# Kernel optimization log

Measured on AMD Instinct MI355X. Metric: run time of the kernel, lower is better.

Reference implementation:

```python
import jax, jax.numpy as jnp
import numpy as np

N_HEAD = 8
DROP_RATE = 0.1


def setup_inputs() -> dict:
    key = jax.random.key(0)
    k1, k2, k3 = jax.random.split(key, 3)
    n, c, h, w = 16, 512, 32, 32
    return {
        "x": jax.random.normal(k1, (n, c, h, w), jnp.float32),
        "qkv_w": jax.random.normal(k2, (3 * c, c), jnp.float32) * 0.02,
        "qkv_b": jnp.zeros((3 * c,), jnp.float32),
        "out_w": jax.random.normal(k3, (c, c), jnp.float32) * 0.02,
        "out_b": jnp.zeros((c,), jnp.float32),
        "dropout_enabled": 0,
    }


def reference(x, qkv_w, qkv_b, out_w, out_b, dropout_enabled):
    n, c, h, w = x.shape
    hd = c // N_HEAD  # head dim
    # fused QKV 1x1 conv == per-pixel matmul: [n, 3c, h, w]
    qkv = jnp.einsum('oc,nchw->nohw', qkv_w, x) + qkv_b[None, :, None, None]
    # [n, 3*n_head, hd, h*w] -> [n, 3*n_head, h*w, hd]
    qkv = jnp.swapaxes(qkv.reshape(n, N_HEAD * 3, hd, h * w), 2, 3)
    q, k, v = jnp.split(qkv, 3, axis=1)  # each [n, n_head, hw, hd]
    scale = hd ** (-0.25)
    att = jax.nn.softmax((q * scale) @ (jnp.swapaxes(k, 2, 3) * scale), axis=3)
    y = jnp.swapaxes(att @ v, 2, 3).reshape(n, c, h, w)
    y = jnp.einsum('oc,nchw->nohw', out_w, y) + out_b[None, :, None, None]
    # Dropout2d: drops whole (n, c) channel maps
    rate = DROP_RATE * dropout_enabled
    keep = jax.random.bernoulli(jax.random.key(42), 1.0 - rate, shape=(n, c))
    y = y * keep[..., None, None] / (1.0 - rate)
    return x + y
```

## Files before the change

kernel.cpp:

```cpp
#include <hip/hip_runtime.h>

typedef short bf16x8 __attribute__((ext_vector_type(8)));
typedef float f32x4 __attribute__((ext_vector_type(4)));
typedef float f32x16 __attribute__((ext_vector_type(16)));

#define MFMA16(a,b,c) __builtin_amdgcn_mfma_f32_16x16x32_bf16((a),(b),(c),0,0,0)
#define MFMA32(a,b,c) __builtin_amdgcn_mfma_f32_32x32x16_bf16((a),(b),(c),0,0,0)

static __device__ __forceinline__ unsigned short f2bf(float f){
  unsigned u; __builtin_memcpy(&u, &f, 4);
  u += 0x7fffu + ((u >> 16) & 1u);
  return (unsigned short)(u >> 16);
}

static __device__ __forceinline__ unsigned cvtpk(float lo, float hi){
  unsigned r;
  asm volatile("v_cvt_pk_bf16_f32 %0, %1, %2" : "=v"(r) : "v"(lo), "v"(hi));
  return r;
}
static __device__ __forceinline__ void pl32swap(unsigned &a, unsigned &b){
  asm volatile("v_permlane32_swap_b32 %0, %1" : "+v"(a), "+v"(b));
}

static __device__ __forceinline__ void gload_lds16(const void* g, void* l) {
  __builtin_amdgcn_global_load_lds(
      (__attribute__((address_space(1))) void*)g,
      (__attribute__((address_space(3))) void*)l, 16, 0, 0);
}

__global__ __launch_bounds__(256) void transpose_cvt(
    const float* __restrict__ in, unsigned short* __restrict__ out,
    const float* __restrict__ qkv_w, const float* __restrict__ out_w,
    unsigned short* __restrict__ wq, unsigned short* __restrict__ wo)
{
  __shared__ unsigned short tile[32][33];
  if (blockIdx.x >= 32) {
    const int b = (blockIdx.x - 32) + 8 * (blockIdx.y + 16 * blockIdx.z);
    const int i = b * 512 + threadIdx.x * 2;
    float2 v; unsigned short* dst;
    if (i < 786432) { v = *(const float2*)&qkv_w[i]; dst = &wq[i]; }
    else { v = *(const float2*)&out_w[i - 786432]; dst = &wo[i - 786432]; }
    dst[0] = f2bf(v.x); dst[1] = f2bf(v.y);
    return;
  }
  const long base = (long)blockIdx.z * 512 * 1024;
  const int t = threadIdx.x, tx = t & 31, ty = t >> 5;
  const int c0 = blockIdx.x * 32, r0 = blockIdx.y * 32;
  const float* ib = in + base;
#pragma unroll
  for (int i = 0; i < 4; ++i)
    tile[ty + i * 8][tx] = f2bf(ib[(long)(r0 + ty + i * 8) * 1024 + c0 + tx]);
  __syncthreads();
  unsigned short* ob = out + base;
#pragma unroll
  for (int i = 0; i < 4; ++i)
    ob[(long)(c0 + ty + i * 8) * 512 + r0 + tx] = tile[tx][ty + i * 8];
}

__global__ __launch_bounds__(256, 2) void gemm_qkv(
    const unsigned short* __restrict__ A, const unsigned short* __restrict__ B,
    unsigned short* __restrict__ qkvout, const float* __restrict__ bias)
{
  const int M = 1024, K = 512;
  __shared__ unsigned short SM[4][128 * 64];
  const int t = threadIdx.x, lane = t & 63, wv = t >> 6;
  const int quad = lane >> 4, ln = lane & 15;

  const int L = blockIdx.x + 12 * blockIdx.y + 96 * blockIdx.z;
  const int v = (L & 7) * 192 + (L >> 3);
  const int m0 = ((v / 12) & 7) * 128, n0 = (v % 12) * 128;
  const long zb = v / 96;
  A += zb * (long)M * K;

  const int srow = wv * 32 + (lane >> 3);
  const int scol = ((lane & 7) * 8) ^ ((lane >> 3) * 8);

  auto stage = [&](int kt, unsigned short* Ad, unsigned short* Bd) {
#pragma unroll
    for (int i = 0; i < 4; ++i) {
      gload_lds16(&A[(long)(m0 + srow + i * 8) * K + kt + scol],
                  &Ad[(wv * 32 + i * 8) * 64]);
      gload_lds16(&B[(long)(n0 + srow + i * 8) * K + kt + scol],
                  &Bd[(wv * 32 + i * 8) * 64]);
    }
  };

  f32x4 zero = {0.f, 0.f, 0.f, 0.f};
  f32x4 acc[4][4];
#pragma unroll
  for (int i = 0; i < 4; ++i)
#pragma unroll
    for (int j = 0; j < 4; ++j) acc[i][j] = zero;

  const int wm = (wv & 1) * 64, wn = (wv >> 1) * 64;
  const int rsw = (ln & 7) * 8;

  stage(0, SM[0], SM[2]);
  __syncthreads();
  for (int kt8 = 0; kt8 < 8; ++kt8) {
    const int cur = kt8 & 1;
    if (kt8 < 7) stage((kt8 + 1) * 64, SM[cur ^ 1], SM[2 + (cur ^ 1)]);
    const unsigned short* As = SM[cur];
    const unsigned short* Bs = SM[2 + cur];
#pragma unroll
    for (int kk = 0; kk < 64; kk += 32) {
      bf16x8 a[4], b[4];
#pragma unroll
      for (int i = 0; i < 4; ++i)
        a[i] = *(const bf16x8*)&As[(wm + i * 16 + ln) * 64 + ((kk + quad * 8) ^ rsw)];
#pragma unroll
      for (int j = 0; j < 4; ++j)
        b[j] = *(const bf16x8*)&Bs[(wn + j * 16 + ln) * 64 + ((kk + quad * 8) ^ rsw)];
#pragma unroll
      for (int i = 0; i < 4; ++i)
#pragma unroll
        for (int j = 0; j < 4; ++j)
          acc[i][j] = MFMA16(a[i], b[j], acc[i][j]);
    }
    __syncthreads();
  }

  const int part = n0 >> 9;
  if (part < 2) {
    const float qs = (part == 0) ? 0.18033688f : 1.0f;
    unsigned short (*T)[136] = (unsigned short(*)[136])&SM[0][0];
#pragma unroll
    for (int j = 0; j < 4; ++j) {
      const int oo = wn + j * 16 + ln;
      const float bb = bias[n0 + oo];
#pragma unroll
      for (int i = 0; i < 4; ++i) {
        const int pp = wm + i * 16 + quad * 4;
        f32x4 vv = acc[i][j];
#pragma unroll
        for (int r = 0; r < 4; ++r)
          T[pp + r][oo] = f2bf((vv[r] + bb) * qs);
      }
    }
    __syncthreads();
    unsigned short* qb = qkvout + (long)part * 8388608;
#pragma unroll
    for (int it = 0; it < 8; ++it) {
      const int idx = it * 256 + t;
      const int p = idx >> 4, c0 = (idx & 15) * 8;
      const int og = n0 + c0;
      const int h = (og >> 6) & 7, d = og & 63;
      bf16x8 val = *(const bf16x8*)&T[p][c0];
      *(bf16x8*)&qb[((long)(zb * 8 + h) * 1024 + m0 + p) * 64 + d] = val;
    }
  } else {
#pragma unroll
    for (int j = 0; j < 4; ++j) {
      const int o = n0 + wn + j * 16 + ln;
      const float bb = bias[o];
#pragma unroll
      for (int i = 0; i < 4; ++i) {
        const int p = m0 + wm + i * 16 + quad * 4;
        const long cidx = ((long)zb * 512 + (o - 1024)) * 1024 + p;
        f32x4 vv = acc[i][j];
        ushort4 st;
        st.x = f2bf(vv[0] + bb); st.y = f2bf(vv[1] + bb);
        st.z = f2bf(vv[2] + bb); st.w = f2bf(vv[3] + bb);
        *(ushort4*)&qkvout[16777216 + cidx] = st;
      }
    }
  }
}

__global__ __launch_bounds__(256, 2) void gemm_out(
    const unsigned short* __restrict__ A, const unsigned short* __restrict__ B,
    float* __restrict__ C, const float* __restrict__ bias,
    const float* __restrict__ xin, const int* __restrict__ de_ptr)
{
  const int M = 1024, K = 512;
  __shared__ unsigned short SM[4][128 * 64];
  const int t = threadIdx.x, lane = t & 63, wv = t >> 6;
  const int quad = lane >> 4, ln = lane & 15;

  const int L = blockIdx.x + 4 * blockIdx.y + 32 * blockIdx.z;
  const int v = (L & 7) * 64 + (L >> 3);
  const int m0 = ((v >> 2) & 7) * 128, n0 = (v & 3) * 128;
  const long zb = v >> 5;
  A += zb * (long)M * K;
  C += zb * 512l * M;
  xin += zb * 512l * M;

  const int srow = wv * 32 + (lane >> 3);
  const int scol = ((lane & 7) * 8) ^ ((lane >> 3) * 8);

  auto stage = [&](int kt, unsigned short* Ad, unsigned short* Bd) {
#pragma unroll
    for (int i = 0; i < 4; ++i) {
      gload_lds16(&A[(long)(m0 + srow + i * 8) * K + kt + scol],
                  &Ad[(wv * 32 + i * 8) * 64]);
      gload_lds16(&B[(long)(n0 + srow + i * 8) * K + kt + scol],
                  &Bd[(wv * 32 + i * 8) * 64]);
    }
  };

  f32x4 zero = {0.f, 0.f, 0.f, 0.f};
  f32x4 acc[4][4];
#pragma unroll
  for (int i = 0; i < 4; ++i)
#pragma unroll
    for (int j = 0; j < 4; ++j) acc[i][j] = zero;

  const int wm = (wv & 1) * 64, wn = (wv >> 1) * 64;
  const int rsw = (ln & 7) * 8;

  stage(0, SM[0], SM[2]);
  __syncthreads();
  for (int kt8 = 0; kt8 < 8; ++kt8) {
    const int cur = kt8 & 1;
    if (kt8 < 7) stage((kt8 + 1) * 64, SM[cur ^ 1], SM[2 + (cur ^ 1)]);
    const unsigned short* As = SM[cur];
    const unsigned short* Bs = SM[2 + cur];
#pragma unroll
    for (int kk = 0; kk < 64; kk += 32) {
      bf16x8 a[4], b[4];
#pragma unroll
      for (int i = 0; i < 4; ++i)
        a[i] = *(const bf16x8*)&As[(wm + i * 16 + ln) * 64 + ((kk + quad * 8) ^ rsw)];
#pragma unroll
      for (int j = 0; j < 4; ++j)
        b[j] = *(const bf16x8*)&Bs[(wn + j * 16 + ln) * 64 + ((kk + quad * 8) ^ rsw)];
#pragma unroll
      for (int i = 0; i < 4; ++i)
#pragma unroll
        for (int j = 0; j < 4; ++j)
          acc[i][j] = MFMA16(a[i], b[j], acc[i][j]);
    }
    __syncthreads();
  }

  float dscale = 1.0f / (1.0f - 0.1f * (float)de_ptr[0]);

#pragma unroll
  for (int j = 0; j < 4; ++j) {
    int o = n0 + wn + j * 16 + ln;
    float bb = bias[o];
#pragma unroll
    for (int i = 0; i < 4; ++i) {
      int p = m0 + wm + i * 16 + quad * 4;
      long cidx = (long)o * M + p;
      f32x4 vv = acc[i][j];
      float4 rx = *(const float4*)&xin[cidx];
      float4 st;
      st.x = rx.x + (vv[0] + bb) * dscale;
      st.y = rx.y + (vv[1] + bb) * dscale;
      st.z = rx.z + (vv[2] + bb) * dscale;
      st.w = rx.w + (vv[3] + bb) * dscale;
      *(float4*)&C[cidx] = st;
    }
  }
}

__global__ __launch_bounds__(512, 2) void attn_kernel(
    const unsigned short* __restrict__ q_pd, const unsigned short* __restrict__ k_pd,
    const unsigned short* __restrict__ v_cp, unsigned short* __restrict__ y_pc)
{
  __shared__ unsigned short Ks[2][128 * 64];
  __shared__ unsigned short Vs[2][64 * 128];
  const int t = threadIdx.x, lane = t & 63, wv = t >> 6;
  const int l31 = lane & 31, bh8 = (lane >> 5) * 8;
  const int qt = blockIdx.y >> 5;
  const int nh = blockIdx.x * 32 + (blockIdx.y & 31);
  const int n = nh >> 3, h = nh & 7;
  const int q0 = qt * 512;

  bf16x8 qa[2][4];
#pragma unroll
  for (int qg = 0; qg < 2; ++qg) {
    const unsigned short* qb =
        q_pd + ((long)nh * 1024 + q0 + wv * 64 + qg * 32 + l31) * 64;
#pragma unroll
    for (int ds = 0; ds < 4; ++ds)
      qa[qg][ds] = *(const bf16x8*)(qb + ds * 16 + bh8);
  }

  f32x16 zacc;
#pragma unroll
  for (int r = 0; r < 16; ++r) zacc[r] = 0.f;
  f32x16 o_acc[2][2];
  o_acc[0][0] = zacc; o_acc[0][1] = zacc; o_acc[1][0] = zacc; o_acc[1][1] = zacc;
  float l_acc[2] = {0.f, 0.f};

  const unsigned short* kg0 = k_pd + (long)nh * 1024 * 64;
  const unsigned short* vg0 = v_cp + ((long)n * 512 + h * 64) * 1024;

  const int krow = lane >> 3;
  const int kcol = ((lane & 7) * 8) ^ ((lane >> 3) * 8);
  const int vrow = lane >> 4;
  const int rsw = (lane & 7) * 8;
  const int vrsw = (l31 & 15) * 8;

  auto stage_kv = [&](int c, int buf) {
    const unsigned short* kg = kg0 + (long)c * 128 * 64;
    const unsigned short* vg = vg0 + c * 128;
    unsigned short* KsD = Ks[buf];
    unsigned short* VsD = Vs[buf];
#pragma unroll
    for (int i = 0; i < 2; ++i) {
      const int vr = ((wv & 1) * 8) + i * 4 + vrow;
      const int vcol = ((lane & 15) ^ vr) * 8;
      gload_lds16(kg + (long)(wv * 16 + i * 8 + krow) * 64 + kcol,
                  &KsD[(wv * 16 + i * 8) * 64]);
      gload_lds16(vg + (long)(wv * 8 + i * 4 + vrow) * 1024 + vcol,
                  &VsD[(wv * 8 + i * 4) * 128]);
    }
  };

  stage_kv(0, 0);

  union U { bf16x8 v; unsigned u[4]; };
  auto sm_pack = [&](const f32x16& sv, bf16x8* paq, float& lac) {
    float e[16];
#pragma unroll
    for (int r = 0; r < 16; ++r) e[r] = __builtin_amdgcn_exp2f(sv[r]);
    float a0 = e[0] + e[1],  a1 = e[2] + e[3],  a2 = e[4] + e[5],  a3 = e[6] + e[7];
    float a4 = e[8] + e[9],  a5 = e[10] + e[11], a6 = e[12] + e[13], a7 = e[14] + e[15];
    float b0 = a0 + a1, b1 = a2 + a3, b2 = a4 + a5, b3 = a6 + a7;
    lac += (b0 + b1) + (b2 + b3);
    unsigned pk4[4][2];
#pragma unroll
    for (int hh = 0; hh < 4; ++hh) {
      pk4[hh][0] = cvtpk(e[4 * hh + 0], e[4 * hh + 1]);
      pk4[hh][1] = cvtpk(e[4 * hh + 2], e[4 * hh + 3]);
    }
#pragma unroll
    for (int hk = 0; hk < 2; ++hk) {
      unsigned x0 = pk4[2 * hk + 1][0], y0 = pk4[2 * hk][0];
      unsigned x1 = pk4[2 * hk + 1][1], y1 = pk4[2 * hk][1];
      pl32swap(x0, y0); pl32swap(x1, y1);
      U u; u.u[0] = y0; u.u[1] = y1; u.u[2] = x0; u.u[3] = x1;
      paq[hk] = u.v;
    }
  };

  auto qk_issue = [&](const unsigned short* KsC, int kgi, f32x16* s) {
    bf16x8 ka[4];
#pragma unroll
    for (int ds = 0; ds < 4; ++ds)
      ka[ds] = *(const bf16x8*)
          &KsC[(kgi * 32 + l31) * 64 + ((ds * 16 + bh8) ^ rsw)];
    s[0] = zacc; s[1] = zacc;
    __builtin_amdgcn_s_setprio(1);
#pragma unroll
    for (int ds = 0; ds < 4; ++ds) {
      s[0] = MFMA32(ka[ds], qa[0][ds], s[0]);
      s[1] = MFMA32(ka[ds], qa[1][ds], s[1]);
    }
    __builtin_amdgcn_s_setprio(0);
  };

  auto body = [&](const unsigned short* KsC, const unsigned short* VsC,
                  int kgi, f32x16* scur, f32x16* snxt) {
    if (kgi < 3) qk_issue(KsC, kgi + 1, snxt);
    bf16x8 va[4];
#pragma unroll
    for (int dg = 0; dg < 2; ++dg)
#pragma unroll
      for (int hk = 0; hk < 2; ++hk)
        va[dg * 2 + hk] = *(const bf16x8*)
            &VsC[(dg * 32 + l31) * 128 + (((kgi * 2 + hk) * 16 + bh8) ^ vrsw)];
    bf16x8 pa[2][2];
    sm_pack(scur[0], pa[0], l_acc[0]);
    sm_pack(scur[1], pa[1], l_acc[1]);
    __builtin_amdgcn_s_setprio(1);
#pragma unroll
    for (int dg = 0; dg < 2; ++dg)
#pragma unroll
      for (int hk = 0; hk < 2; ++hk) {
        o_acc[dg][0] = MFMA32(va[dg * 2 + hk], pa[0][hk], o_acc[dg][0]);
        o_acc[dg][1] = MFMA32(va[dg * 2 + hk], pa[1][hk], o_acc[dg][1]);
      }
    __builtin_amdgcn_s_setprio(0);
  };

  for (int c = 0; c < 8; ++c) {
    const int cur = c & 1;
    if (c < 7) {
      stage_kv(c + 1, cur ^ 1);
      asm volatile("s_waitcnt vmcnt(4)" ::: "memory");
    } else {
      asm volatile("s_waitcnt vmcnt(0)" ::: "memory");
    }
    __builtin_amdgcn_s_barrier();
    const unsigned short* KsC = Ks[cur];
    const unsigned short* VsC = Vs[cur];

    f32x16 sA[2], sB[2];
    qk_issue(KsC, 0, sA);
    body(KsC, VsC, 0, sA, sB);
    body(KsC, VsC, 1, sB, sA);
    body(KsC, VsC, 2, sA, sB);
    body(KsC, VsC, 3, sB, sA);

    __builtin_amdgcn_s_barrier();
  }

#pragma unroll
  for (int qg = 0; qg < 2; ++qg) {
    float la = l_acc[qg];
    la += __shfl_xor(la, 32);
    float linv = 1.0f / la;
    const int q = q0 + wv * 64 + qg * 32 + l31;
    unsigned short* yb = y_pc + ((long)n * 1024 + q) * 512 + h * 64;
#pragma unroll
    for (int dg = 0; dg < 2; ++dg) {
      f32x16 o = o_acc[dg][qg];
#pragma unroll
      for (int rq = 0; rq < 4; ++rq) {
        int d0 = dg * 32 + rq * 8 + (bh8 >> 1);
        ushort4 st;
        st.x = f2bf(o[rq * 4 + 0] * linv);
        st.y = f2bf(o[rq * 4 + 1] * linv);
        st.z = f2bf(o[rq * 4 + 2] * linv);
        st.w = f2bf(o[rq * 4 + 3] * linv);
        *(ushort4*)&yb[d0] = st;
      }
    }
  }
}

extern "C" void kernel_launch(void* const* d_in, const int* in_sizes, int n_in,
                              void* d_out, int out_size, void* d_ws, size_t ws_size,
                              hipStream_t stream) {
  (void)in_sizes; (void)n_in; (void)out_size; (void)ws_size;
  const float* x     = (const float*)d_in[0];
  const float* qkv_w = (const float*)d_in[1];
  const float* qkv_b = (const float*)d_in[2];
  const float* out_w = (const float*)d_in[3];
  const float* out_b = (const float*)d_in[4];
  const int* de = (const int*)d_in[5];
  float* out = (float*)d_out;
  unsigned short* ws = (unsigned short*)d_ws;

  unsigned short* xT   = ws;
  unsigned short* qkv  = ws + 8388608;
  unsigned short* y_pc = ws;
  unsigned short* wq   = ws + 33554432;
  unsigned short* wo   = wq + 786432;

  transpose_cvt<<<dim3(40, 16, 16), 256, 0, stream>>>(
      x, xT, qkv_w, out_w, wq, wo);

  gemm_qkv<<<dim3(12, 8, 16), 256, 0, stream>>>(xT, wq, qkv, qkv_b);

  attn_kernel<<<dim3(4, 64), 512, 0, stream>>>(
      qkv, qkv + 8388608, qkv + 16777216, y_pc);

  gemm_out<<<dim3(4, 8, 16), 256, 0, stream>>>(
      y_pc, wo, out, out_b, x, de);
}
```

Measured before the change: 181.8 us.

## Load K/V straight from global into registers, drop LDS staging, remap blocks per XCD

The attention kernel stops staging K and V tiles through double-buffered shared memory with barriers. Each wave now loads its K and V fragments directly from global memory into registers, prefetching the next K chunk one step ahead. Blocks shrink to 256 threads covering 256 queries, and the 1D grid is mapped so the blocks for one head land on the same XCD, which should improve L2 reuse of K/V. This removes LDS traffic and barrier stalls, but each wave reloads K/V from cache, which raises global/L2 traffic and exposes load latency without the barrier-synchronised pipeline.

```diff
diff --git a/kernel.cpp b/kernel.cpp
--- a/kernel.cpp
+++ b/kernel.cpp
@@ -255,18 +255,18 @@
   }
 }
 
-__global__ __launch_bounds__(512, 2) void attn_kernel(
+__global__ __launch_bounds__(256, 2) void attn_kernel(
     const unsigned short* __restrict__ q_pd, const unsigned short* __restrict__ k_pd,
     const unsigned short* __restrict__ v_cp, unsigned short* __restrict__ y_pc)
 {
-  __shared__ unsigned short Ks[2][128 * 64];
-  __shared__ unsigned short Vs[2][64 * 128];
   const int t = threadIdx.x, lane = t & 63, wv = t >> 6;
   const int l31 = lane & 31, bh8 = (lane >> 5) * 8;
-  const int qt = blockIdx.y >> 5;
-  const int nh = blockIdx.x * 32 + (blockIdx.y & 31);
+  const int bid = blockIdx.x;
+  const int xcd = bid & 7, idx = bid >> 3;
+  const int nh = xcd * 16 + (idx & 15);
+  const int qt = idx >> 4;
   const int n = nh >> 3, h = nh & 7;
-  const int q0 = qt * 512;
+  const int q0 = qt * 256;
 
   bf16x8 qa[2][4];
 #pragma unroll
@@ -285,32 +285,22 @@
   o_acc[0][0] = zacc; o_acc[0][1] = zacc; o_acc[1][0] = zacc; o_acc[1][1] = zacc;
   float l_acc[2] = {0.f, 0.f};
 
-  const unsigned short* kg0 = k_pd + (long)nh * 1024 * 64;
-  const unsigned short* vg0 = v_cp + ((long)n * 512 + h * 64) * 1024;
-
-  const int krow = lane >> 3;
-  const int kcol = ((lane & 7) * 8) ^ ((lane >> 3) * 8);
-  const int vrow = lane >> 4;
-  const int rsw = (lane & 7) * 8;
-  const int vrsw = (l31 & 15) * 8;
-
-  auto stage_kv = [&](int c, int buf) {
-    const unsigned short* kg = kg0 + (long)c * 128 * 64;
-    const unsigned short* vg = vg0 + c * 128;
-    unsigned short* KsD = Ks[buf];
-    unsigned short* VsD = Vs[buf];
-#pragma unroll
-    for (int i = 0; i < 2; ++i) {
-      const int vr = ((wv & 1) * 8) + i * 4 + vrow;
-      const int vcol = ((lane & 15) ^ vr) * 8;
-      gload_lds16(kg + (long)(wv * 16 + i * 8 + krow) * 64 + kcol,
-                  &KsD[(wv * 16 + i * 8) * 64]);
-      gload_lds16(vg + (long)(wv * 8 + i * 4 + vrow) * 1024 + vcol,
-                  &VsD[(wv * 8 + i * 4) * 128]);
-    }
-  };
-
-  stage_kv(0, 0);
+  const unsigned short* kp = k_pd + (long)nh * 1024 * 64 + (long)l31 * 64 + bh8;
+  const unsigned short* vp0 = v_cp + ((long)n * 512 + h * 64 + l31) * 1024 + bh8;
+  const unsigned short* vp1 = vp0 + 32l * 1024;
+
+  auto load_k = [&](int kb, bf16x8* ka) {
+    const unsigned short* p = kp + (long)kb * 64;
+#pragma unroll
+    for (int ds = 0; ds < 4; ++ds)
+      ka[ds] = *(const bf16x8*)(p + ds * 16);
+  };
+  auto load_v = [&](int kb, bf16x8* va) {
+    va[0] = *(const bf16x8*)(vp0 + kb);
+    va[1] = *(const bf16x8*)(vp0 + kb + 16);
+    va[2] = *(const bf16x8*)(vp1 + kb);
+    va[3] = *(const bf16x8*)(vp1 + kb + 16);
+  };
 
   union U { bf16x8 v; unsigned u[4]; };
   auto sm_pack = [&](const f32x16& sv, bf16x8* paq, float& lac) {
@@ -337,35 +327,21 @@
     }
   };
 
-  auto qk_issue = [&](const unsigned short* KsC, int kgi, f32x16* s) {
-    bf16x8 ka[4];
-#pragma unroll
-    for (int ds = 0; ds < 4; ++ds)
-      ka[ds] = *(const bf16x8*)
-          &KsC[(kgi * 32 + l31) * 64 + ((ds * 16 + bh8) ^ rsw)];
-    s[0] = zacc; s[1] = zacc;
+  auto step = [&](int kb, bf16x8* kcur, bf16x8* knxt) {
+    if (kb + 32 < 1024) load_k(kb + 32, knxt);
+    bf16x8 va[4];
+    load_v(kb, va);
+    f32x16 s0 = zacc, s1 = zacc;
     __builtin_amdgcn_s_setprio(1);
 #pragma unroll
     for (int ds = 0; ds < 4; ++ds) {
-      s[0] = MFMA32(ka[ds], qa[0][ds], s[0]);
-      s[1] = MFMA32(ka[ds], qa[1][ds], s[1]);
+      s0 = MFMA32(kcur[ds], qa[0][ds], s0);
+      s1 = MFMA32(kcur[ds], qa[1][ds], s1);
     }
     __builtin_amdgcn_s_setprio(0);
-  };
-
-  auto body = [&](const unsigned short* KsC, const unsigned short* VsC,
-                  int kgi, f32x16* scur, f32x16* snxt) {
-    if (kgi < 3) qk_issue(KsC, kgi + 1, snxt);
-    bf16x8 va[4];
-#pragma unroll
-    for (int dg = 0; dg < 2; ++dg)
-#pragma unroll
-      for (int hk = 0; hk < 2; ++hk)
-        va[dg * 2 + hk] = *(const bf16x8*)
-            &VsC[(dg * 32 + l31) * 128 + (((kgi * 2 + hk) * 16 + bh8) ^ vrsw)];
     bf16x8 pa[2][2];
-    sm_pack(scur[0], pa[0], l_acc[0]);
-    sm_pack(scur[1], pa[1], l_acc[1]);
+    sm_pack(s0, pa[0], l_acc[0]);
+    sm_pack(s1, pa[1], l_acc[1]);
     __builtin_amdgcn_s_setprio(1);
 #pragma unroll
     for (int dg = 0; dg < 2; ++dg)
@@ -377,26 +353,11 @@
     __builtin_amdgcn_s_setprio(0);
   };
 
-  for (int c = 0; c < 8; ++c) {
-    const int cur = c & 1;
-    if (c < 7) {
-      stage_kv(c + 1, cur ^ 1);
-      asm volatile("s_waitcnt vmcnt(4)" ::: "memory");
-    } else {
-      asm volatile("s_waitcnt vmcnt(0)" ::: "memory");
-    }
-    __builtin_amdgcn_s_barrier();
-    const unsigned short* KsC = Ks[cur];
-    const unsigned short* VsC = Vs[cur];
-
-    f32x16 sA[2], sB[2];
-    qk_issue(KsC, 0, sA);
-    body(KsC, VsC, 0, sA, sB);
-    body(KsC, VsC, 1, sB, sA);
-    body(KsC, VsC, 2, sA, sB);
-    body(KsC, VsC, 3, sB, sA);
-
-    __builtin_amdgcn_s_barrier();
+  bf16x8 kaA[4], kaB[4];
+  load_k(0, kaA);
+  for (int kb = 0; kb < 1024; kb += 64) {
+    step(kb, kaA, kaB);
+    step(kb + 32, kaB, kaA);
   }
 
 #pragma unroll
@@ -447,7 +408,7 @@
 
   gemm_qkv<<<dim3(12, 8, 16), 256, 0, stream>>>(xT, wq, qkv, qkv_b);
 
-  attn_kernel<<<dim3(4, 64), 512, 0, stream>>>(
+  attn_kernel<<<512, 256, 0, stream>>>(
       qkv, qkv + 8388608, qkv + 16777216, y_pc);
 
   gemm_out<<<dim3(4, 8, 16), 256, 0, stream>>>(
```

Result: slower. 207.0 us (+13.8%).
